# Kernel optimization log

Hardware: AMD Instinct MI355X
Metric: run time of the kernel (lower is better)

Reference implementation:

```python
import jax, jax.numpy as jnp
import numpy as np

N = 50000
E = 800000
IN_C = 512
HID = 256
OUT_C = 2
NUM_LAYERS = 3
NUM_HIER = 3
EPS = 1e-5


def setup_inputs() -> dict:
    key = jax.random.key(0)
    ks = jax.random.split(key, 24)
    g = lambda k, shp, fan: jax.random.normal(k, shp, jnp.float32) / np.sqrt(fan)
    inp = {
        "x": jax.random.normal(ks[0], (N, IN_C), jnp.float32),
        "edge_index": jax.random.randint(ks[1], (2, E), 0, N, jnp.int64),
        # GCN conv weights/biases
        "conv_w0": g(ks[2], (IN_C, HID), IN_C),
        "conv_ws": g(ks[3], (NUM_LAYERS - 1, HID, HID), HID),
        "conv_b": jnp.zeros((NUM_LAYERS, HID), jnp.float32),
        "bn_g": jnp.ones((NUM_LAYERS, HID), jnp.float32),
        "bn_b": jnp.zeros((NUM_LAYERS, HID), jnp.float32),
        # global-path MLPs
        "fcg_w0": g(ks[4], (HID, HID), HID),
        "fcg_ws": g(ks[5], (NUM_HIER - 1, 2 * HID, HID), 2 * HID),
        "fcg_b": jnp.zeros((NUM_HIER, HID), jnp.float32),
        "bng_g": jnp.ones((NUM_HIER, HID), jnp.float32),
        "bng_b": jnp.zeros((NUM_HIER, HID), jnp.float32),
        # local-path MLPs
        "fcl_w": g(ks[6], (NUM_HIER, HID, HID), HID),
        "fcl_b": jnp.zeros((NUM_HIER, HID), jnp.float32),
        "bnl_g": jnp.ones((NUM_HIER, HID), jnp.float32),
        "bnl_b": jnp.zeros((NUM_HIER, HID), jnp.float32),
        # output heads
        "outg_w": g(ks[7], (HID, OUT_C), HID),
        "outg_b": jnp.zeros((OUT_C,), jnp.float32),
        "outl_w": g(ks[8], (NUM_HIER, HID, OUT_C), HID),
        "outl_b": jnp.zeros((NUM_HIER, OUT_C), jnp.float32),
    }
    return inp


def _gcn_edges(edge_index):
    # add self-loops, compute symmetric normalization D^-1/2 (A+I) D^-1/2
    loops = jnp.arange(N, dtype=edge_index.dtype)
    rows = jnp.concatenate([edge_index[0], loops])
    cols = jnp.concatenate([edge_index[1], loops])
    deg = jax.ops.segment_sum(jnp.ones_like(rows, jnp.float32), rows, num_segments=N)
    dinv = jnp.where(deg > 0, jax.lax.rsqrt(deg), 0.0)
    w = dinv[rows] * dinv[cols]
    return rows, cols, w


def _propagate(h, rows, cols, w):
    msg = h[cols] * w[:, None]          # [E+N, HID] gather
    return jax.ops.segment_sum(msg, rows, num_segments=N)


def _bn(h, gamma, beta):
    m = h.mean(0)
    v = h.var(0)
    return gamma * (h - m) * jax.lax.rsqrt(v + EPS) + beta


def reference(x, edge_index, conv_w0, conv_ws, conv_b, bn_g, bn_b,
              fcg_w0, fcg_ws, fcg_b, bng_g, bng_b,
              fcl_w, fcl_b, bnl_g, bnl_b,
              outg_w, outg_b, outl_w, outl_b):
    rows, cols, ew = _gcn_edges(edge_index)
    h = x
    for i in range(NUM_LAYERS):
        W = conv_w0 if i == 0 else conv_ws[i - 1]
        h = _propagate(h @ W, rows, cols, ew) + conv_b[i]
        h = jax.nn.relu(_bn(h, bn_g[i], bn_b[i]))  # dropout = identity (eval)
    # hierarchical global path
    hg = []
    xg = jax.nn.relu(_bn(h @ fcg_w0 + fcg_b[0], bng_g[0], bng_b[0]))
    hg.append(xg)
    for i in range(NUM_HIER - 1):
        xg = jnp.concatenate([hg[i], h], -1) @ fcg_ws[i] + fcg_b[i + 1]
        xg = jax.nn.relu(_bn(xg, bng_g[i + 1], bng_b[i + 1]))
        hg.append(xg)
    og = jax.nn.log_softmax(hg[-1] @ outg_w + outg_b, axis=-1)
    # local heads
    ol = []
    for i in range(NUM_HIER):
        hl = jax.nn.relu(_bn(hg[i] @ fcl_w[i] + fcl_b[i], bnl_g[i], bnl_b[i]))
        ol.append(jax.nn.log_softmax(hl @ outl_w[i] + outl_b[i], axis=-1))
    # stack: [1 + NUM_HIER, N, OUT_C] (og first, then local heads)
    return jnp.stack([og] + ol, axis=0)
```

## Files before the change

kernel.cpp:

```cpp
#include <hip/hip_runtime.h>
#include <math.h>

#define N_NODES 50000
#define E_EDGES 800000
#define HID 256
#define EPS_BN 1e-5f

#define AGG_BPS 256

#define SCAN_CHUNK 1024
#define SCAN_NCH ((N_NODES + SCAN_CHUNK - 1) / SCAN_CHUNK)

typedef __attribute__((ext_vector_type(8))) short short8;
typedef __attribute__((ext_vector_type(4))) float floatx4;
typedef __attribute__((ext_vector_type(8))) unsigned short ushort8v;

__device__ __forceinline__ unsigned short f2bf(float f) {
    unsigned u = __float_as_uint(f);
    u = (u + 0x7FFFu + ((u >> 16) & 1u)) >> 16;
    return (unsigned short)u;
}
__device__ __forceinline__ float bf2f(unsigned short b) {
    return __uint_as_float(((unsigned)b) << 16);
}
__device__ __forceinline__ void bn_scsh(const float* stats, const float* gamma,
                                        const float* beta, int ch,
                                        float& sc, float& sh) {
    const float invn = 1.0f / (float)N_NODES;
    float mean = stats[ch] * invn;
    float var = stats[HID + ch] * invn - mean * mean;
    var = fmaxf(var, 0.f);
    sc = gamma[ch] * rsqrtf(var + EPS_BN);
    sh = beta[ch] - mean * sc;
}

__global__ __launch_bounds__(256) void k_deg(const int* __restrict__ rows,
                                             int* __restrict__ deg) {
    int e = blockIdx.x * 256 + threadIdx.x;
    atomicAdd(&deg[rows[e]], 1);
}

__global__ __launch_bounds__(256) void k_dinv(const int* __restrict__ deg,
                                              float* __restrict__ dinv) {
    int n = blockIdx.x * 256 + threadIdx.x;
    if (n < N_NODES) dinv[n] = rsqrtf((float)deg[n] + 1.0f);
}

__global__ __launch_bounds__(1024) void k_scan1(const int* __restrict__ deg,
                                                int* __restrict__ rowptr,
                                                int* __restrict__ bsum) {
    __shared__ int wsum[16];
    int tid = threadIdx.x, lane = tid & 63, w = tid >> 6;
    int idx = blockIdx.x * SCAN_CHUNK + tid;
    int v = (idx < N_NODES) ? deg[idx] : 0;
    int x = v;
#pragma unroll
    for (int d = 1; d < 64; d <<= 1) {
        int t = __shfl_up(x, d);
        if (lane >= d) x += t;
    }
    if (lane == 63) wsum[w] = x;
    __syncthreads();
    if (w == 0) {
        int ws = (lane < 16) ? wsum[lane] : 0;
#pragma unroll
        for (int d = 1; d < 16; d <<= 1) {
            int t = __shfl_up(ws, d);
            if (lane >= d) ws += t;
        }
        if (lane < 16) wsum[lane] = ws;
    }
    __syncthreads();
    int wbase = (w > 0) ? wsum[w - 1] : 0;
    if (idx < N_NODES) rowptr[idx] = wbase + x - v;
    if (tid == 0) bsum[blockIdx.x] = wsum[15];
}
__global__ __launch_bounds__(64) void k_scan2(const int* __restrict__ bsum,
                                              int* __restrict__ boff) {
    int lane = threadIdx.x;
    int v = (lane < SCAN_NCH) ? bsum[lane] : 0;
    int x = v;
#pragma unroll
    for (int d = 1; d < 64; d <<= 1) {
        int t = __shfl_up(x, d);
        if (lane >= d) x += t;
    }
    if (lane < SCAN_NCH) boff[lane] = x - v;
    if (lane == SCAN_NCH - 1) boff[SCAN_NCH] = x;
}
__global__ __launch_bounds__(1024) void k_scan3(int* __restrict__ rowptr,
                                                const int* __restrict__ boff) {
    int idx = blockIdx.x * SCAN_CHUNK + threadIdx.x;
    if (idx < N_NODES) rowptr[idx] += boff[blockIdx.x];
    if (blockIdx.x == 0 && threadIdx.x == 0) rowptr[N_NODES] = boff[SCAN_NCH];
}

__global__ __launch_bounds__(256) void k_fill(const int* __restrict__ rows,
                                              const int* __restrict__ cols,
                                              const int* __restrict__ rowptr,
                                              int* __restrict__ cursor,
                                              int* __restrict__ colidx) {
    int e = blockIdx.x * 256 + threadIdx.x;
    int r = rows[e];
    int pos = atomicAdd(&cursor[r], 1);
    colidx[rowptr[r] + pos] = cols[e];
}

__global__ __launch_bounds__(256) void k_f2bf_slice(const float* __restrict__ X,
                                                    unsigned short* __restrict__ Y) {
    int i = blockIdx.x * 256 + threadIdx.x;
    int slice = i / (N_NODES * 4);
    int rem = i - slice * (N_NODES * 4);
    int node = rem >> 2, p8 = rem & 3;
    const float* xp = X + (size_t)node * 512 + slice * 32 + p8 * 8;
    float4 va = ((const float4*)xp)[0];
    float4 vb = ((const float4*)xp)[1];
    ushort8v o;
    o[0] = f2bf(va.x); o[1] = f2bf(va.y); o[2] = f2bf(va.z); o[3] = f2bf(va.w);
    o[4] = f2bf(vb.x); o[5] = f2bf(vb.y); o[6] = f2bf(vb.z); o[7] = f2bf(vb.w);
    *(ushort8v*)(Y + (size_t)i * 8) = o;
}

__global__ __launch_bounds__(256) void k_wt(const float* __restrict__ W,
                                            unsigned short* __restrict__ Wt,
                                            int K, int total) {
    int idx = blockIdx.x * 256 + threadIdx.x;
    if (idx >= total) return;
    int KS = K << 8;
    int m = idx / KS;
    int rel = idx - m * KS;
    int k = rel >> 8;
    int n = rel & 255;
    Wt[(size_t)m * KS + (size_t)n * K + k] = f2bf(W[idx]);
}

__global__ __launch_bounds__(256) void k_gemm_mfma(
    const unsigned short* __restrict__ A0,
    const unsigned short* __restrict__ A1, int K0, int K,
    const unsigned short* __restrict__ Bt,
    unsigned short* __restrict__ C,
    const float* __restrict__ rowscale,
    float* __restrict__ stats)
{
    __shared__ alignas(16) unsigned char smem[36864];
    unsigned short* AsB = (unsigned short*)smem;
    unsigned short* BsB = (unsigned short*)(smem + 16384);
    int tid = threadIdx.x;
    int wid = tid >> 6, lane = tid & 63;
    int row0 = blockIdx.x * 128;
    int n0 = blockIdx.y * 128;
    int wrow = (wid & 1) * 64, wcol = (wid >> 1) * 64;
    int lr = lane >> 2;
    int lk = (lane & 3) * 8;
    int qq = lane >> 4, mr = lane & 15;

    floatx4 acc[4][4];
#pragma unroll
    for (int i = 0; i < 4; ++i)
#pragma unroll
        for (int j = 0; j < 4; ++j) {
            floatx4 z = {0.f, 0.f, 0.f, 0.f};
            acc[i][j] = z;
        }

    for (int k0 = 0; k0 < K; k0 += 64) {
#pragma unroll
        for (int h = 0; h < 2; ++h) {
            int kk = k0 + h * 32;
            const unsigned short* Abase =
                (kk < K0) ? A0 + (size_t)(kk >> 5) * (N_NODES * 32)
                          : A1 + (size_t)((kk - K0) >> 5) * (N_NODES * 32);
#pragma unroll
            for (int i = 0; i < 2; ++i) {
                int rloc = wid * 32 + i * 16 + lr;
                int grow = row0 + rloc;
                if (grow > N_NODES - 1) grow = N_NODES - 1;
                const unsigned short* gp = Abase + (size_t)grow * 32 + lk;
                unsigned short* l = AsB + h * 4096 + (wid * 32 + i * 16) * 32;
                __builtin_amdgcn_global_load_lds(
                    (const __attribute__((address_space(1))) void*)gp,
                    (__attribute__((address_space(3))) void*)l, 16, 0, 0);
            }
#pragma unroll
            for (int i = 0; i < 2; ++i) {
                int nloc = wid * 32 + i * 16 + lr;
                const unsigned short* gp = Bt + (size_t)(n0 + nloc) * K + kk + lk;
                unsigned short* l = BsB + h * 4096 + (wid * 32 + i * 16) * 32;
                __builtin_amdgcn_global_load_lds(
                    (const __attribute__((address_space(1))) void*)gp,
                    (__attribute__((address_space(3))) void*)l, 16, 0, 0);
            }
        }
        __syncthreads();
#pragma unroll
        for (int h = 0; h < 2; ++h) {
            short8 af[4], bfv[4];
#pragma unroll
            for (int i = 0; i < 4; ++i)
                af[i] = *(const short8*)(AsB + h * 4096 + (wrow + i * 16 + mr) * 32 + qq * 8);
#pragma unroll
            for (int j = 0; j < 4; ++j)
                bfv[j] = *(const short8*)(BsB + h * 4096 + (wcol + j * 16 + mr) * 32 + qq * 8);
#pragma unroll
            for (int i = 0; i < 4; ++i)
#pragma unroll
                for (int j = 0; j < 4; ++j)
                    acc[i][j] = __builtin_amdgcn_mfma_f32_16x16x32_bf16(
                        af[i], bfv[j], acc[i][j], 0, 0, 0);
        }
        __syncthreads();
    }

    unsigned short* lds_c = (unsigned short*)smem;
    float* ls = (float*)(smem + 34816);
    float* lq = ls + 128;
    if (stats) ((float*)(smem + 34816))[tid] = 0.f;

    float psum[4] = {0.f, 0.f, 0.f, 0.f};
    float psq[4]  = {0.f, 0.f, 0.f, 0.f};
#pragma unroll
    for (int i = 0; i < 4; ++i) {
        int trow_base = wrow + i * 16 + qq * 4;
#pragma unroll
        for (int r = 0; r < 4; ++r) {
            int trow = trow_base + r;
            int grow = row0 + trow;
            bool rok = grow < N_NODES;
            float rs = 1.0f;
            if (rowscale && rok) rs = rowscale[grow];
#pragma unroll
            for (int j = 0; j < 4; ++j) {
                float v = acc[i][j][r] * rs;
                lds_c[trow * 136 + wcol + j * 16 + mr] = f2bf(v);
                if (rok) { psum[j] += v; psq[j] += v * v; }
            }
        }
    }
    __syncthreads();
    if (stats) {
#pragma unroll
        for (int j = 0; j < 4; ++j) {
            int lc = wcol + j * 16 + mr;
            atomicAdd(&ls[lc], psum[j]);
            atomicAdd(&lq[lc], psq[j]);
        }
    }
    int rowlim = N_NODES - row0; if (rowlim > 128) rowlim = 128;
    int sbase = n0 >> 5;
#pragma unroll
    for (int u = 0; u < 8; ++u) {
        int uid = tid + 256 * u;
        int row = uid >> 4;
        int q = (uid >> 2) & 3;
        int sub = uid & 3;
        if (row < rowlim) {
            ushort8v vv = *(const ushort8v*)(lds_c + row * 136 + q * 32 + sub * 8);
            *(ushort8v*)(C + ((size_t)(sbase + q) * N_NODES + row0 + row) * 32 + sub * 8) = vv;
        }
    }
    if (stats) {
        __syncthreads();
        if (tid < 128) atomicAdd(&stats[n0 + tid], ls[tid]);
        else atomicAdd(&stats[HID + n0 + (tid - 128)], lq[tid - 128]);
    }
}

__global__ __launch_bounds__(256) void k_aggregate_bf(
    const unsigned short* __restrict__ g,
    unsigned short* __restrict__ outp,
    const int* __restrict__ rowptr,
    const int* __restrict__ colidx,
    const float* __restrict__ dinv,
    float* __restrict__ stats) {
    int lane = threadIdx.x & 63;
    int wid = threadIdx.x >> 6;
    int slice = blockIdx.x & 7;
    int bslice = blockIdx.x >> 3;
    const unsigned short* gs = g + (size_t)slice * (N_NODES * 32);
    unsigned short* os = outp + (size_t)slice * (N_NODES * 32);
    int g8 = lane >> 3;
    int l8 = lane & 7;
    int wavebase = (bslice * 4 + wid) * 8;
    const int stride = AGG_BPS * 4 * 8;

    float sa0 = 0.f, sa1 = 0.f, sa2 = 0.f, sa3 = 0.f;
    float qa0 = 0.f, qa1 = 0.f, qa2 = 0.f, qa3 = 0.f;

    for (int nb = wavebase; nb < N_NODES; nb += stride) {
        int node = nb + g8;
        bool valid = node < N_NODES;
        int nc = valid ? node : N_NODES - 1;
        int s = rowptr[nc];
        int e = valid ? rowptr[nc + 1] : s;
        int e1 = e - 1;
        auto cl = [&](int j) { int t = j < e1 ? j : e1; return t > 0 ? t : 0; };

        ushort4 sv = *(const ushort4*)(gs + ((size_t)nc << 5) + (l8 << 2));
        float rs = dinv[nc];
        float a0 = bf2f(sv.x), a1 = bf2f(sv.y), a2 = bf2f(sv.z), a3 = bf2f(sv.w);

        int cn0 = colidx[cl(s)], cn1 = colidx[cl(s + 1)];
        ushort4 vn0 = *(const ushort4*)(gs + ((size_t)cn0 << 5) + (l8 << 2));
        ushort4 vn1 = *(const ushort4*)(gs + ((size_t)cn1 << 5) + (l8 << 2));
        cn0 = colidx[cl(s + 2)];
        cn1 = colidx[cl(s + 3)];

        for (int i = s; i < e; i += 2) {
            ushort4 u0 = vn0, u1 = vn1;
            vn0 = *(const ushort4*)(gs + ((size_t)cn0 << 5) + (l8 << 2));
            vn1 = *(const ushort4*)(gs + ((size_t)cn1 << 5) + (l8 << 2));
            cn0 = colidx[cl(i + 4)];
            cn1 = colidx[cl(i + 5)];
            float m1 = (i + 1 < e) ? 1.f : 0.f;
            a0 += bf2f(u0.x); a1 += bf2f(u0.y);
            a2 += bf2f(u0.z); a3 += bf2f(u0.w);
            a0 = fmaf(m1, bf2f(u1.x), a0); a1 = fmaf(m1, bf2f(u1.y), a1);
            a2 = fmaf(m1, bf2f(u1.z), a2); a3 = fmaf(m1, bf2f(u1.w), a3);
        }
        if (valid) {
            float r0 = a0 * rs, r1 = a1 * rs, r2 = a2 * rs, r3 = a3 * rs;
            ushort4 o;
            o.x = f2bf(r0); o.y = f2bf(r1); o.z = f2bf(r2); o.w = f2bf(r3);
            union { ushort4 u4; unsigned long long u64; } cvt;
            cvt.u4 = o;
            __builtin_nontemporal_store(
                cvt.u64, (unsigned long long*)(os + ((size_t)node << 5) + (l8 << 2)));
            sa0 += r0; sa1 += r1; sa2 += r2; sa3 += r3;
            qa0 += r0 * r0; qa1 += r1 * r1; qa2 += r2 * r2; qa3 += r3 * r3;
        }
    }
#pragma unroll
    for (int off = 8; off < 64; off <<= 1) {
        sa0 += __shfl_xor(sa0, off); sa1 += __shfl_xor(sa1, off);
        sa2 += __shfl_xor(sa2, off); sa3 += __shfl_xor(sa3, off);
        qa0 += __shfl_xor(qa0, off); qa1 += __shfl_xor(qa1, off);
        qa2 += __shfl_xor(qa2, off); qa3 += __shfl_xor(qa3, off);
    }
    __shared__ float ls[32], lq[32];
    if (threadIdx.x < 32) { ls[threadIdx.x] = 0.f; lq[threadIdx.x] = 0.f; }
    __syncthreads();
    if (lane < 8) {
        atomicAdd(&ls[l8 * 4 + 0], sa0); atomicAdd(&lq[l8 * 4 + 0], qa0);
        atomicAdd(&ls[l8 * 4 + 1], sa1); atomicAdd(&lq[l8 * 4 + 1], qa1);
        atomicAdd(&ls[l8 * 4 + 2], sa2); atomicAdd(&lq[l8 * 4 + 2], qa2);
        atomicAdd(&ls[l8 * 4 + 3], sa3); atomicAdd(&lq[l8 * 4 + 3], qa3);
    }
    __syncthreads();
    if (threadIdx.x < 32) {
        atomicAdd(&stats[slice * 32 + threadIdx.x], ls[threadIdx.x]);
        atomicAdd(&stats[HID + slice * 32 + threadIdx.x], lq[threadIdx.x]);
    }
}

__global__ __launch_bounds__(256) void k_bnapply_bf(const unsigned short* __restrict__ X,
                                                    unsigned short* __restrict__ Y,
                                                    const float* __restrict__ stats,
                                                    const float* __restrict__ gamma,
                                                    const float* __restrict__ beta) {
    __shared__ float s_sc[64], s_sh[64];
    int i = blockIdx.x * 256 + threadIdx.x;
    int slice_lo = (blockIdx.x * 256) / (N_NODES * 4);
    int slice_hi = (blockIdx.x * 256 + 255) / (N_NODES * 4);
    if (threadIdx.x < 64) {
        int half = threadIdx.x >> 5;
        int c = threadIdx.x & 31;
        int sl = half ? slice_hi : slice_lo;
        float sc, sh;
        bn_scsh(stats, gamma, beta, sl * 32 + c, sc, sh);
        s_sc[threadIdx.x] = sc; s_sh[threadIdx.x] = sh;
    }
    __syncthreads();
    int slice = i / (N_NODES * 4);
    int sel = (slice != slice_lo) ? 32 : 0;
    int c8 = sel + (i & 3) * 8;
    ushort8v v = *(const ushort8v*)(X + (size_t)i * 8);
    ushort8v o;
#pragma unroll
    for (int k = 0; k < 8; ++k) {
        float f = bf2f((unsigned short)v[k]);
        o[k] = f2bf(fmaxf(f * s_sc[c8 + k] + s_sh[c8 + k], 0.f));
    }
    *(ushort8v*)(Y + (size_t)i * 8) = o;
}

__global__ __launch_bounds__(256) void k_head_bf(const unsigned short* __restrict__ H,
                                                 const float* __restrict__ stats,
                                                 const float* __restrict__ gamma,
                                                 const float* __restrict__ beta,
                                                 const float* __restrict__ W,
                                                 const float* __restrict__ b,
                                                 float* __restrict__ outp) {
    __shared__ float h_sc[HID], h_sh[HID];
    if (stats) {
        float sc, sh;
        bn_scsh(stats, gamma, beta, threadIdx.x, sc, sh);
        h_sc[threadIdx.x] = sc; h_sh[threadIdx.x] = sh;
    }
    __syncthreads();
    int wave = (blockIdx.x * 256 + threadIdx.x) >> 6;
    int lane = threadIdx.x & 63;
    if (wave >= N_NODES) return;
    ushort4 h4 = *(const ushort4*)(
        H + ((size_t)(lane >> 3) * N_NODES + wave) * 32 + (lane & 7) * 4);
    float h0 = bf2f(h4.x), h1 = bf2f(h4.y), h2 = bf2f(h4.z), h3 = bf2f(h4.w);
    if (stats) {
        int ch = lane * 4;
        h0 = fmaxf(h0 * h_sc[ch + 0] + h_sh[ch + 0], 0.f);
        h1 = fmaxf(h1 * h_sc[ch + 1] + h_sh[ch + 1], 0.f);
        h2 = fmaxf(h2 * h_sc[ch + 2] + h_sh[ch + 2], 0.f);
        h3 = fmaxf(h3 * h_sc[ch + 3] + h_sh[ch + 3], 0.f);
    }
    const float2* W2 = (const float2*)W;
    float2 w0 = W2[lane * 4 + 0], w1 = W2[lane * 4 + 1];
    float2 w2 = W2[lane * 4 + 2], w3 = W2[lane * 4 + 3];
    float p0 = h0 * w0.x + h1 * w1.x + h2 * w2.x + h3 * w3.x;
    float p1 = h0 * w0.y + h1 * w1.y + h2 * w2.y + h3 * w3.y;
    for (int off = 32; off > 0; off >>= 1) {
        p0 += __shfl_down(p0, off);
        p1 += __shfl_down(p1, off);
    }
    if (lane == 0) {
        float z0 = p0 + b[0], z1 = p1 + b[1];
        float m = fmaxf(z0, z1);
        float lse = m + logf(expf(z0 - m) + expf(z1 - m));
        outp[(size_t)wave * 2 + 0] = z0 - lse;
        outp[(size_t)wave * 2 + 1] = z1 - lse;
    }
}

extern "C" void kernel_launch(void* const* d_in, const int* in_sizes, int n_in,
                              void* d_out, int out_size, void* d_ws, size_t ws_size,
                              hipStream_t stream) {
    const float* x       = (const float*)d_in[0];
    const int*   ei      = (const int*)d_in[1];
    const float* conv_w0 = (const float*)d_in[2];
    const float* conv_ws = (const float*)d_in[3];
    const float* bn_g    = (const float*)d_in[5];
    const float* bn_b    = (const float*)d_in[6];
    const float* fcg_w0  = (const float*)d_in[7];
    const float* fcg_ws  = (const float*)d_in[8];
    const float* bng_g   = (const float*)d_in[10];
    const float* bng_b   = (const float*)d_in[11];
    const float* fcl_w   = (const float*)d_in[12];
    const float* bnl_g   = (const float*)d_in[14];
    const float* bnl_b   = (const float*)d_in[15];
    const float* outg_w  = (const float*)d_in[16];
    const float* outg_b  = (const float*)d_in[17];
    const float* outl_w  = (const float*)d_in[18];
    const float* outl_b  = (const float*)d_in[19];
    float* out = (float*)d_out;

    const int* rows = ei;
    const int* cols = ei + E_EDGES;

    char* ws = (char*)d_ws;
    size_t off = 0;
    auto carve = [&](size_t bytes) -> void* {
        void* p = ws + off;
        off = (off + bytes + 255) & ~(size_t)255;
        return p;
    };
    const size_t ACT = (size_t)N_NODES * HID * 2;
    unsigned short* xbf = (unsigned short*)carve((size_t)N_NODES * 512 * 2);
    unsigned short* tG  = (unsigned short*)carve(ACT);
    unsigned short* tA  = (unsigned short*)carve(ACT);
    unsigned short* hbf = (unsigned short*)carve(ACT);
    unsigned short* g1  = (unsigned short*)carve(ACT);
    unsigned short* g2  = (unsigned short*)carve(ACT);
    unsigned short* wt_conv0 = (unsigned short*)carve(256 * 512 * 2);
    unsigned short* wt_conv1 = (unsigned short*)carve(256 * 256 * 2);
    unsigned short* wt_conv2 = (unsigned short*)carve(256 * 256 * 2);
    unsigned short* wt_fcg0  = (unsigned short*)carve(256 * 256 * 2);
    unsigned short* wt_fcgs0 = (unsigned short*)carve(256 * 512 * 2);
    unsigned short* wt_fcgs1 = (unsigned short*)carve(256 * 512 * 2);
    unsigned short* wt_fcl0  = (unsigned short*)carve(256 * 256 * 2);
    unsigned short* wt_fcl1  = (unsigned short*)carve(256 * 256 * 2);
    unsigned short* wt_fcl2  = (unsigned short*)carve(256 * 256 * 2);
    int*   deg    = (int*)carve(2 * 50048 * 4);
    int*   cursor = deg + 50048;
    int*   rowptr = (int*)carve((size_t)(N_NODES + 1) * 4);
    float* dinv   = (float*)carve((size_t)N_NODES * 4);
    int*   colidx = (int*)carve((size_t)E_EDGES * 4);
    float* stats_all = (float*)carve(9 * 2 * HID * 4);
    int*   scanbuf = (int*)carve(512);
    int*   bsum = scanbuf;
    int*   boff = scanbuf + 64;
    (void)off; (void)ws_size; (void)in_sizes; (void)n_in; (void)out_size;

    hipMemsetAsync(deg, 0, 2 * 50048 * 4, stream);
    hipMemsetAsync(stats_all, 0, 9 * 2 * HID * 4, stream);
    k_deg<<<E_EDGES / 256, 256, 0, stream>>>(rows, deg);
    k_dinv<<<(N_NODES + 255) / 256, 256, 0, stream>>>(deg, dinv);
    k_scan1<<<SCAN_NCH, 1024, 0, stream>>>(deg, rowptr, bsum);
    k_scan2<<<1, 64, 0, stream>>>(bsum, boff);
    k_scan3<<<SCAN_NCH, 1024, 0, stream>>>(rowptr, boff);
    k_fill<<<E_EDGES / 256, 256, 0, stream>>>(rows, cols, rowptr, cursor, colidx);

    k_f2bf_slice<<<N_NODES * 64 / 256, 256, 0, stream>>>(x, xbf);
    k_wt<<<(512 * 256 + 255) / 256, 256, 0, stream>>>(conv_w0, wt_conv0, 512, 512 * 256);
    k_wt<<<(2 * 256 * 256 + 255) / 256, 256, 0, stream>>>(conv_ws, wt_conv1, 256, 2 * 256 * 256);
    k_wt<<<(256 * 256 + 255) / 256, 256, 0, stream>>>(fcg_w0, wt_fcg0, 256, 256 * 256);
    k_wt<<<(2 * 512 * 256 + 255) / 256, 256, 0, stream>>>(fcg_ws, wt_fcgs0, 512, 2 * 512 * 256);
    k_wt<<<(3 * 256 * 256 + 255) / 256, 256, 0, stream>>>(fcl_w, wt_fcl0, 256, 3 * 256 * 256);

    dim3 ggrid((N_NODES + 127) / 128, 2);
    auto gemm = [&](const unsigned short* A0, const unsigned short* A1,
                    int K0, int K, const unsigned short* Bt, unsigned short* C,
                    const float* rs, float* st) {
        k_gemm_mfma<<<ggrid, 256, 0, stream>>>(A0, A1, K0, K, Bt, C, rs, st);
    };
    auto bnapply = [&](float* st, const unsigned short* X, unsigned short* Y,
                       const float* gamma, const float* beta) {
        k_bnapply_bf<<<N_NODES * 32 / 256, 256, 0, stream>>>(X, Y, st, gamma, beta);
    };
    auto agg = [&](const unsigned short* in, unsigned short* outb, float* st) {
        k_aggregate_bf<<<8 * AGG_BPS, 256, 0, stream>>>(in, outb, rowptr, colidx,
                                                        dinv, st);
    };
    float* st;

    st = stats_all + 0 * 512;
    gemm(xbf, nullptr, 512, 512, wt_conv0, tG, dinv, nullptr);
    agg(tG, tA, st);
    bnapply(st, tA, g1, bn_g + 0, bn_b + 0);
    st = stats_all + 1 * 512;
    gemm(g1, nullptr, 256, 256, wt_conv1, tG, dinv, nullptr);
    agg(tG, tA, st);
    bnapply(st, tA, g2, bn_g + 256, bn_b + 256);
    st = stats_all + 2 * 512;
    gemm(g2, nullptr, 256, 256, wt_conv2, tG, dinv, nullptr);
    agg(tG, tA, st);
    bnapply(st, tA, hbf, bn_g + 512, bn_b + 512);

    st = stats_all + 3 * 512;
    gemm(hbf, nullptr, 256, 256, wt_fcg0, tG, nullptr, st);
    bnapply(st, tG, g1, bng_g + 0, bng_b + 0);
    st = stats_all + 4 * 512;
    gemm(g1, nullptr, 256, 256, wt_fcl0, tG, nullptr, st);
    k_head_bf<<<N_NODES / 4, 256, 0, stream>>>(tG, st, bnl_g + 0, bnl_b + 0,
                                               outl_w, outl_b,
                                               out + (size_t)1 * N_NODES * 2);
    st = stats_all + 5 * 512;
    gemm(g1, hbf, 256, 512, wt_fcgs0, tG, nullptr, st);
    bnapply(st, tG, g2, bng_g + 256, bng_b + 256);
    st = stats_all + 6 * 512;
    gemm(g2, nullptr, 256, 256, wt_fcl1, tG, nullptr, st);
    k_head_bf<<<N_NODES / 4, 256, 0, stream>>>(tG, st, bnl_g + 256, bnl_b + 256,
                                               outl_w + 512, outl_b + 2,
                                               out + (size_t)2 * N_NODES * 2);
    st = stats_all + 7 * 512;
    gemm(g2, hbf, 256, 512, wt_fcgs1, tG, nullptr, st);
    bnapply(st, tG, g1, bng_g + 512, bng_b + 512);
    st = stats_all + 8 * 512;
    gemm(g1, nullptr, 256, 256, wt_fcl2, tG, nullptr, st);
    k_head_bf<<<N_NODES / 4, 256, 0, stream>>>(tG, st, bnl_g + 512, bnl_b + 512,
                                               outl_w + 1024, outl_b + 4,
                                               out + (size_t)3 * N_NODES * 2);
    k_head_bf<<<N_NODES / 4, 256, 0, stream>>>(g1, nullptr, nullptr, nullptr,
                                               outg_w, outg_b, out);
}
```

Baseline: 928.3 us.

## Double-buffer GEMM LDS tiles to overlap next K-chunk loads with MFMA

```diff
diff --git a/kernel.cpp b/kernel.cpp
--- a/kernel.cpp
+++ b/kernel.cpp
@@ -143,8 +143,7 @@
     float* __restrict__ stats)
 {
     __shared__ alignas(16) unsigned char smem[36864];
-    unsigned short* AsB = (unsigned short*)smem;
-    unsigned short* BsB = (unsigned short*)(smem + 16384);
+    unsigned short* sbase = (unsigned short*)smem;
     int tid = threadIdx.x;
     int wid = tid >> 6, lane = tid & 63;
     int row0 = blockIdx.x * 128;
@@ -163,51 +162,57 @@
             acc[i][j] = z;
         }
 
-    for (int k0 = 0; k0 < K; k0 += 64) {
-#pragma unroll
-        for (int h = 0; h < 2; ++h) {
-            int kk = k0 + h * 32;
-            const unsigned short* Abase =
-                (kk < K0) ? A0 + (size_t)(kk >> 5) * (N_NODES * 32)
-                          : A1 + (size_t)((kk - K0) >> 5) * (N_NODES * 32);
-#pragma unroll
-            for (int i = 0; i < 2; ++i) {
-                int rloc = wid * 32 + i * 16 + lr;
-                int grow = row0 + rloc;
-                if (grow > N_NODES - 1) grow = N_NODES - 1;
-                const unsigned short* gp = Abase + (size_t)grow * 32 + lk;
-                unsigned short* l = AsB + h * 4096 + (wid * 32 + i * 16) * 32;
-                __builtin_amdgcn_global_load_lds(
-                    (const __attribute__((address_space(1))) void*)gp,
-                    (__attribute__((address_space(3))) void*)l, 16, 0, 0);
-            }
-#pragma unroll
-            for (int i = 0; i < 2; ++i) {
-                int nloc = wid * 32 + i * 16 + lr;
-                const unsigned short* gp = Bt + (size_t)(n0 + nloc) * K + kk + lk;
-                unsigned short* l = BsB + h * 4096 + (wid * 32 + i * 16) * 32;
-                __builtin_amdgcn_global_load_lds(
-                    (const __attribute__((address_space(1))) void*)gp,
-                    (__attribute__((address_space(3))) void*)l, 16, 0, 0);
-            }
-        }
-        __syncthreads();
-#pragma unroll
-        for (int h = 0; h < 2; ++h) {
-            short8 af[4], bfv[4];
-#pragma unroll
-            for (int i = 0; i < 4; ++i)
-                af[i] = *(const short8*)(AsB + h * 4096 + (wrow + i * 16 + mr) * 32 + qq * 8);
+    int KL = K >> 5;
+
+    auto stage = [&](int c, int b) {
+        int kk = c << 5;
+        const unsigned short* Abase =
+            (kk < K0) ? A0 + (size_t)(kk >> 5) * (N_NODES * 32)
+                      : A1 + (size_t)((kk - K0) >> 5) * (N_NODES * 32);
+        unsigned short* Adst = sbase + b * 4096;
+        unsigned short* Bdst = sbase + 8192 + b * 4096;
+#pragma unroll
+        for (int i = 0; i < 2; ++i) {
+            int rloc = wid * 32 + i * 16 + lr;
+            int grow = row0 + rloc;
+            if (grow > N_NODES - 1) grow = N_NODES - 1;
+            const unsigned short* gp = Abase + (size_t)grow * 32 + lk;
+            unsigned short* l = Adst + (wid * 32 + i * 16) * 32;
+            __builtin_amdgcn_global_load_lds(
+                (const __attribute__((address_space(1))) void*)gp,
+                (__attribute__((address_space(3))) void*)l, 16, 0, 0);
+        }
+#pragma unroll
+        for (int i = 0; i < 2; ++i) {
+            int nloc = wid * 32 + i * 16 + lr;
+            const unsigned short* gp = Bt + (size_t)(n0 + nloc) * K + kk + lk;
+            unsigned short* l = Bdst + (wid * 32 + i * 16) * 32;
+            __builtin_amdgcn_global_load_lds(
+                (const __attribute__((address_space(1))) void*)gp,
+                (__attribute__((address_space(3))) void*)l, 16, 0, 0);
+        }
+    };
+
+    stage(0, 0);
+    __syncthreads();
+    for (int c = 0; c < KL; ++c) {
+        int cur = c & 1;
+        if (c + 1 < KL) stage(c + 1, cur ^ 1);
+        const unsigned short* Asrc = sbase + cur * 4096;
+        const unsigned short* Bsrc = sbase + 8192 + cur * 4096;
+        short8 af[4], bfv[4];
+#pragma unroll
+        for (int i = 0; i < 4; ++i)
+            af[i] = *(const short8*)(Asrc + (wrow + i * 16 + mr) * 32 + qq * 8);
+#pragma unroll
+        for (int j = 0; j < 4; ++j)
+            bfv[j] = *(const short8*)(Bsrc + (wcol + j * 16 + mr) * 32 + qq * 8);
+#pragma unroll
+        for (int i = 0; i < 4; ++i)
 #pragma unroll
             for (int j = 0; j < 4; ++j)
-                bfv[j] = *(const short8*)(BsB + h * 4096 + (wcol + j * 16 + mr) * 32 + qq * 8);
-#pragma unroll
-            for (int i = 0; i < 4; ++i)
-#pragma unroll
-                for (int j = 0; j < 4; ++j)
-                    acc[i][j] = __builtin_amdgcn_mfma_f32_16x16x32_bf16(
-                        af[i], bfv[j], acc[i][j], 0, 0, 0);
-        }
+                acc[i][j] = __builtin_amdgcn_mfma_f32_16x16x32_bf16(
+                    af[i], bfv[j], acc[i][j], 0, 0, 0);
         __syncthreads();
     }
 
@@ -246,7 +251,7 @@
         }
     }
     int rowlim = N_NODES - row0; if (rowlim > 128) rowlim = 128;
-    int sbase = n0 >> 5;
+    int sbase_n = n0 >> 5;
 #pragma unroll
     for (int u = 0; u < 8; ++u) {
         int uid = tid + 256 * u;
@@ -255,7 +260,7 @@
         int sub = uid & 3;
         if (row < rowlim) {
             ushort8v vv = *(const ushort8v*)(lds_c + row * 136 + q * 32 + sub * 8);
-            *(ushort8v*)(C + ((size_t)(sbase + q) * N_NODES + row0 + row) * 32 + sub * 8) = vv;
+            *(ushort8v*)(C + ((size_t)(sbase_n + q) * N_NODES + row0 + row) * 32 + sub * 8) = vv;
         }
     }
     if (stats) {
```

After: 931.6 us. No clear change (+0.4%).
